# Optimization experiments

Measured on AMD Instinct MI355X. Metric: run time of the kernel, lower is better.

The kernel has to match this reference:

```python
import jax, jax.numpy as jnp
import numpy as np

N_NODES = 50000
IN_CH = 128
OUT_CH = 64
HID = 2 * OUT_CH  # 128
N_EDGES = 800000


def _glorot(key, shape):
    fan_in, fan_out = shape[0], shape[-1]
    lim = jnp.sqrt(6.0 / (fan_in + fan_out))
    return jax.random.uniform(key, shape, jnp.float32, -lim, lim)


def setup_inputs() -> dict:
    key = jax.random.key(0)
    ks = jax.random.split(key, 10)
    x = jax.random.normal(ks[0], (N_NODES, IN_CH), jnp.float32)
    edge_index = jax.random.randint(ks[1], (2, N_EDGES), 0, N_NODES, jnp.int32)
    return {
        "x": x,
        "edge_index": edge_index,
        "W1": _glorot(ks[2], (IN_CH, HID)),
        "a_src1": _glorot(ks[3], (HID,)),
        "a_dst1": _glorot(ks[4], (HID,)),
        "b1": jnp.zeros((HID,), jnp.float32),
        "W2": _glorot(ks[5], (HID, OUT_CH)),
        "a_src2": _glorot(ks[6], (OUT_CH,)),
        "a_dst2": _glorot(ks[7], (OUT_CH,)),
        "b2": jnp.zeros((OUT_CH,), jnp.float32),
    }


def _gat_conv(x, src, dst, W, a_src, a_dst, b, n_nodes):
    # Linear transform: [N, F_out]
    h = x @ W
    # Per-node attention halves (heads=1): alpha_i = <h_i, a>
    al_s = h @ a_src  # [N]
    al_d = h @ a_dst  # [N]
    # Edge scores with LeakyReLU(0.2), PyG default negative slope
    e = jax.nn.leaky_relu(al_s[src] + al_d[dst], negative_slope=0.2)
    # Segment softmax over incoming edges of each dst node
    m = jax.ops.segment_max(e, dst, num_segments=n_nodes)
    m = jnp.where(jnp.isfinite(m), m, 0.0)
    ex = jnp.exp(e - m[dst])
    denom = jax.ops.segment_sum(ex, dst, num_segments=n_nodes)
    alpha = ex / (denom[dst] + 1e-16)  # [E]
    # Weighted scatter-add aggregation
    out = jax.ops.segment_sum(h[src] * alpha[:, None], dst, num_segments=n_nodes)
    return out + b


def reference(x, edge_index, W1, a_src1, a_dst1, b1, W2, a_src2, a_dst2, b2):
    n = x.shape[0]
    # add_self_loops=True (PyG GATConv default)
    loops = jnp.arange(n, dtype=edge_index.dtype)
    src = jnp.concatenate([edge_index[0], loops])
    dst = jnp.concatenate([edge_index[1], loops])
    h = _gat_conv(x.astype(jnp.float32), src, dst, W1, a_src1, a_dst1, b1, n)
    h = jax.nn.relu(h)
    return _gat_conv(h, src, dst, W2, a_src2, a_dst2, b2, n)
```

## Files before the change

kernel.cpp:

```cpp
#include <hip/hip_runtime.h>
#include <hip/hip_bf16.h>

#define N_NODES 50000
#define IN_CH 128
#define HID 128
#define OUT_CH 64
#define N_EDGES 800000
#define N_TOT_EDGES (N_EDGES + N_NODES)
#define ET_PAD (N_TOT_EDGES + 3 * N_NODES)
#define MPAD 50048
#define NBN ((N_NODES + 255) / 256)
#define NB_E ((N_EDGES + 255) / 256)
#define NB_ET ((N_TOT_EDGES + 255) / 256)
#define NB_GEMM (MPAD / 64)
#define NB8 ((8 * N_NODES + 255) / 256)

typedef float float4v __attribute__((ext_vector_type(4)));
typedef unsigned uint4v __attribute__((ext_vector_type(4)));
typedef __attribute__((ext_vector_type(8))) short bf16x8;
typedef __attribute__((ext_vector_type(4))) float f32x4;

__device__ __forceinline__ unsigned bf16_rne(float f) {
    unsigned u = __float_as_uint(f);
    return (u + 0x7fffu + ((u >> 16) & 1u)) >> 16;
}
__device__ __forceinline__ unsigned pack2(float a, float b) {
    return bf16_rne(a) | (bf16_rne(b) << 16);
}

__global__ __launch_bounds__(256) void k_pre(
        int* __restrict__ cnt8,
        const float* __restrict__ W1, unsigned short* __restrict__ Wl1,
        const float* __restrict__ W2, unsigned short* __restrict__ Wl2) {
    const int b = blockIdx.x, t = threadIdx.x;
    if (b < NB8) {
        int i = b * 256 + t;
        if (i < 8 * N_NODES) cnt8[i] = 0;
        return;
    }
    const float* W; unsigned short* Wl; int N, bb;
    if (b < NB8 + 8) { W = W1; Wl = Wl1; N = 128; bb = b - NB8; }
    else             { W = W2; Wl = Wl2; N = 64;  bb = b - NB8 - 8; }
    const int tg = bb * 256 + t;
    if (tg >= 16 * N) return;
    const int kg = tg / N, col = tg & (N - 1);
    float v[8];
    #pragma unroll
    for (int j = 0; j < 8; ++j) v[j] = W[(size_t)(kg * 8 + j) * N + col];
    uint4 p;
    p.x = pack2(v[0], v[1]); p.y = pack2(v[2], v[3]);
    p.z = pack2(v[4], v[5]); p.w = pack2(v[6], v[7]);
    *(uint4*)&Wl[(size_t)tg * 8] = p;
}


__device__ __forceinline__ void count_body(int b, int t,
        const int* __restrict__ dst_row, int* __restrict__ cnt8,
        unsigned short* __restrict__ rank, int e) {
    int i = b * 256 + t;
    if (i < e) {
        int d = __builtin_nontemporal_load(&dst_row[i]);
        int c = b & 7;
        rank[i] = (unsigned short)atomicAdd(&cnt8[c * N_NODES + d], 1);
    }
}

template<int N, bool AF32, bool USELDS>
__device__ __forceinline__ void gemm_body(int gb, int t,
        const float* __restrict__ Xf, const unsigned short* __restrict__ Xb,
        const unsigned short* __restrict__ Wlg,
        const float* __restrict__ asrc, const float* __restrict__ adst,
        unsigned short* __restrict__ Hb, float* __restrict__ als,
        float* __restrict__ ald, int M, unsigned short* Wl) {
    constexpr int NF = N / 16;
    const unsigned short* Wsrc;
    if constexpr (USELDS) {
        for (int i = t; i < N * 16; i += 256)
            ((uint4*)Wl)[i] = ((const uint4*)Wlg)[i];
        __syncthreads();
        Wsrc = Wl;
    } else {
        Wsrc = Wlg;
    }

    const int lane = t & 63, w = t >> 6;
    const int rb = gb * 64 + w * 16;
    const int cl = lane & 15, g = lane >> 4;

    f32x4 acc[NF];
    #pragma unroll
    for (int n = 0; n < NF; ++n) acc[n] = (f32x4){0.f, 0.f, 0.f, 0.f};

    const float* Xrow = nullptr;
    const unsigned short* Abase = nullptr;
    if constexpr (AF32) {
        const int arow = (rb + cl < M) ? (rb + cl) : (M - 1);
        Xrow = Xf + (size_t)arow * 128;
    } else {
        Abase = Xb + (size_t)(rb >> 4) * 2048 + cl * 8;
    }

    #pragma unroll
    for (int s = 0; s < 4; ++s) {
        bf16x8 af;
        if constexpr (AF32) {
            const int k0 = (s * 4 + g) * 8;
            float4 a = *(const float4*)&Xrow[k0];
            float4 c = *(const float4*)&Xrow[k0 + 4];
            uint4v uu;
            uu[0] = pack2(a.x, a.y); uu[1] = pack2(a.z, a.w);
            uu[2] = pack2(c.x, c.y); uu[3] = pack2(c.z, c.w);
            af = __builtin_bit_cast(bf16x8, uu);
        } else {
            af = *(const bf16x8*)(Abase + (s * 4 + g) * 128);
        }
        #pragma unroll
        for (int n = 0; n < NF; ++n) {
            bf16x8 bf = *(const bf16x8*)(Wsrc + ((s * 4 + g) * N + n * 16 + cl) * 8);
            acc[n] = __builtin_amdgcn_mfma_f32_16x16x32_bf16(af, bf, acc[n], 0, 0, 0);
        }
    }

    float asv[NF], adv[NF];
    #pragma unroll
    for (int n = 0; n < NF; ++n) {
        asv[n] = asrc[n * 16 + cl];
        adv[n] = adst[n * 16 + cl];
    }

    #pragma unroll
    for (int r = 0; r < 4; ++r) {
        float ps = 0.f, pd = 0.f;
        #pragma unroll
        for (int n = 0; n < NF; ++n) {
            ps += acc[n][r] * asv[n];
            pd += acc[n][r] * adv[n];
        }
        #pragma unroll
        for (int mask = 1; mask < 16; mask <<= 1) {
            ps += __shfl_xor(ps, mask);
            pd += __shfl_xor(pd, mask);
        }
        const int row = rb + g * 4 + r;
        if (cl == 0 && row < M) { als[row] = ps; ald[row] = pd; }
    }

    #pragma unroll
    for (int r = 0; r < 4; ++r) {
        const int row = rb + g * 4 + r;
        if (row >= M) continue;
        #pragma unroll
        for (int n = 0; n < NF; ++n)
            Hb[(size_t)(n >> 1) * (size_t)M * 32 + (size_t)row * 32
               + (n & 1) * 16 + cl] = (unsigned short)bf16_rne(acc[n][r]);
    }
}

__global__ __launch_bounds__(256) void k_par1(
        const int* __restrict__ ei, int* __restrict__ cnt8,
        unsigned short* __restrict__ rank,
        const float* __restrict__ X, const unsigned short* __restrict__ Wl1,
        const float* __restrict__ asrc, const float* __restrict__ adst,
        unsigned short* __restrict__ Hb, float* __restrict__ als,
        float* __restrict__ ald, int M) {
    const int b = blockIdx.x, t = threadIdx.x;
    if (b < NB_E) { count_body(b, t, ei + N_EDGES, cnt8, rank, N_EDGES); return; }
    gemm_body<HID, true, false>(b - NB_E, t, X, nullptr, Wl1,
                                asrc, adst, Hb, als, ald, M, nullptr);
}

__global__ void k_scan1(const int* __restrict__ cnt8, int* __restrict__ cntT,
                        unsigned short* __restrict__ pcoff,
                        int* __restrict__ off, int* __restrict__ bsum, int n) {
    __shared__ int s[256];
    int t = threadIdx.x;
    int i = blockIdx.x * 256 + t;
    int padded = 0;
    if (i < n) {
        int pc = 1;
        unsigned short po[8];
        #pragma unroll
        for (int c = 0; c < 8; ++c) {
            po[c] = (unsigned short)pc;
            pc += cnt8[c * n + i];
        }
        cntT[i] = pc;
        uint4 p;
        p.x = (unsigned)po[0] | ((unsigned)po[1] << 16);
        p.y = (unsigned)po[2] | ((unsigned)po[3] << 16);
        p.z = (unsigned)po[4] | ((unsigned)po[5] << 16);
        p.w = (unsigned)po[6] | ((unsigned)po[7] << 16);
        *(uint4*)&pcoff[(size_t)i * 8] = p;
        padded = (pc + 3) & ~3;
    }
    s[t] = padded;
    __syncthreads();
    for (int d = 1; d < 256; d <<= 1) {
        int x = (t >= d) ? s[t - d] : 0;
        __syncthreads();
        s[t] += x;
        __syncthreads();
    }
    if (i < n) off[i + 1] = s[t];
    if (t == 255) bsum[blockIdx.x] = s[255];
}

__global__ void k_scan3(int* __restrict__ off, const int* __restrict__ bsum, int n) {
    __shared__ int s[256];
    int t = threadIdx.x;
    s[t] = (t < NBN) ? bsum[t] : 0;
    __syncthreads();
    for (int d = 1; d < 256; d <<= 1) {
        int x = (t >= d) ? s[t - d] : 0;
        __syncthreads();
        s[t] += x;
        __syncthreads();
    }
    int base = (blockIdx.x > 0) ? s[blockIdx.x - 1] : 0;
    int i = blockIdx.x * 256 + t;
    if (i < n) off[i + 1] += base;
    if (i == 0) off[0] = 0;
}

__global__ void k_fill2(const int* __restrict__ ei, const int* __restrict__ off,
                        const unsigned short* __restrict__ rank,
                        const unsigned short* __restrict__ pcoff,
                        int* __restrict__ csr, int e, int n) {
    int i = blockIdx.x * 256 + threadIdx.x;
    if (i < e) {
        int src = __builtin_nontemporal_load(&ei[i]);
        int dst = __builtin_nontemporal_load(&ei[e + i]);
        int c = (i >> 8) & 7;
        int pos = off[dst] + (int)pcoff[(size_t)dst * 8 + c] + (int)rank[i];
        csr[pos] = src;
    } else if (i < e + n) {
        int v = i - e;
        csr[off[v]] = v;
    }
}

__global__ __launch_bounds__(256) void gemm_mfma64(
        const unsigned short* __restrict__ Xb, const unsigned short* __restrict__ Wlg,
        const float* __restrict__ asrc, const float* __restrict__ adst,
        unsigned short* __restrict__ Hb, float* __restrict__ als,
        float* __restrict__ ald, int M) {
    __shared__ unsigned short Wl[16 * 64 * 8];
    gemm_body<OUT_CH, false, true>(blockIdx.x, threadIdx.x, nullptr, Xb, Wlg,
                                   asrc, adst, Hb, als, ald, M, Wl);
}

template<bool PADZ>
__global__ __launch_bounds__(256) void k_edgew(
        const float* __restrict__ als, const float* __restrict__ ald,
        const int* __restrict__ off, const int* __restrict__ cntT,
        const int* __restrict__ csr,
        unsigned* __restrict__ ew, float* __restrict__ invden, int n) {
    const int fl = threadIdx.x & 15;
    const int v = blockIdx.x * 16 + (threadIdx.x >> 4);
    if (v >= n) return;
    const int start = off[v], end = start + cntT[v];
    const float aldv = ald[v];
    float s = 0.f;
    for (int j = start + fl; j < end; j += 16) {
        int src = __builtin_nontemporal_load(&csr[j]);
        float e = als[src] + aldv;
        e = e > 0.f ? e : 0.2f * e;
        unsigned r = bf16_rne(__expf(e));
        ew[j] = ((unsigned)src << 16) | r;
        s += __uint_as_float(r << 16);
    }
    if (PADZ) {
        const int pend = off[v + 1];
        for (int j = end + fl; j < pend; j += 16) ew[j] = 0;
    }
    #pragma unroll
    for (int d = 1; d < 16; d <<= 1) s += __shfl_xor(s, d);
    if (fl == 0) invden[v] = 1.f / (s + 1e-16f);
}

template<int F, bool RELU, bool PACKOUT>
__global__ __launch_bounds__(256) void k_spmm_b(
        const unsigned short* __restrict__ Hb, const unsigned* __restrict__ ew,
        const float* __restrict__ invden, const float* __restrict__ bias,
        const int* __restrict__ off, void* __restrict__ outv, int n) {
    constexpr int NCH = F / 32;
    const int chunk = blockIdx.x % NCH;
    const int v = (blockIdx.x / NCH) * 64 + (threadIdx.x >> 2);
    if (v >= n) return;
    const int q = threadIdx.x & 3;
    const int start = off[v], end = off[v + 1];
    const unsigned short* __restrict__ Hch = Hb + (size_t)chunk * (size_t)n * 32 + q * 8;

    float a0[8] = {}, a1[8] = {}, a2[8] = {}, a3[8] = {};

    #define GATB(E, A)                                                   \
        {                                                                \
            float w_ = __uint_as_float((E) << 16);                       \
            uint4 h_ = *(const uint4*)&Hch[(size_t)((E) >> 16) * 32];    \
            A[0] += w_ * __uint_as_float(h_.x << 16);                    \
            A[1] += w_ * __uint_as_float(h_.x & 0xffff0000u);            \
            A[2] += w_ * __uint_as_float(h_.y << 16);                    \
            A[3] += w_ * __uint_as_float(h_.y & 0xffff0000u);            \
            A[4] += w_ * __uint_as_float(h_.z << 16);                    \
            A[5] += w_ * __uint_as_float(h_.z & 0xffff0000u);            \
            A[6] += w_ * __uint_as_float(h_.w << 16);                    \
            A[7] += w_ * __uint_as_float(h_.w & 0xffff0000u);            \
        }
    #define GATB4(Q) GATB((Q).x, a0) GATB((Q).y, a1) GATB((Q).z, a2) GATB((Q).w, a3)

    int j = start;
    for (; j + 4 < end; j += 8) {
        uint4 eA = *(const uint4*)&ew[j];
        uint4 eB = *(const uint4*)&ew[j + 4];
        GATB4(eA)
        GATB4(eB)
    }
    if (j < end) {
        uint4 eA = *(const uint4*)&ew[j];
        GATB4(eA)
    }
    #undef GATB4
    #undef GATB

    const float inv = invden[v];
    const float* __restrict__ bp = bias + chunk * 32 + q * 8;
    float s[8];
    #pragma unroll
    for (int i = 0; i < 8; ++i) {
        s[i] = (a0[i] + a1[i] + a2[i] + a3[i]) * inv + bp[i];
        if (RELU) s[i] = fmaxf(s[i], 0.f);
    }

    if (PACKOUT) {
        unsigned short* Xb2 = (unsigned short*)outv;
        const int kg = chunk * 4 + q;
        uint4v p;
        p[0] = pack2(s[0], s[1]); p[1] = pack2(s[2], s[3]);
        p[2] = pack2(s[4], s[5]); p[3] = pack2(s[6], s[7]);
        __builtin_nontemporal_store(p,
            (uint4v*)&Xb2[(size_t)(v >> 4) * 2048 + kg * 128 + (v & 15) * 8]);
    } else {
        float* out = (float*)outv;
        float4v o0, o1;
        o0[0] = s[0]; o0[1] = s[1]; o0[2] = s[2]; o0[3] = s[3];
        o1[0] = s[4]; o1[1] = s[5]; o1[2] = s[6]; o1[3] = s[7];
        float* op = out + (size_t)v * F + chunk * 32 + q * 8;
        __builtin_nontemporal_store(o0, (float4v*)op);
        __builtin_nontemporal_store(o1, (float4v*)(op + 4));
    }
}


extern "C" void kernel_launch(void* const* d_in, const int* in_sizes, int n_in,
                              void* d_out, int out_size, void* d_ws, size_t ws_size,
                              hipStream_t stream) {
    const float* x     = (const float*)d_in[0];
    const int*   ei    = (const int*)d_in[1];
    const float* W1    = (const float*)d_in[2];
    const float* as1   = (const float*)d_in[3];
    const float* ad1   = (const float*)d_in[4];
    const float* b1    = (const float*)d_in[5];
    const float* W2    = (const float*)d_in[6];
    const float* as2   = (const float*)d_in[7];
    const float* ad2   = (const float*)d_in[8];
    const float* b2    = (const float*)d_in[9];
    float* out = (float*)d_out;

    const int Nn = N_NODES;

    char* ws = (char*)d_ws;
    size_t o = 0;
    auto carve = [&](size_t bytes) { char* p = ws + o; o = (o + bytes + 255) & ~(size_t)255; return p; };
    int*            off  = (int*)carve((Nn + 1) * sizeof(int));
    int*            cnt8 = (int*)carve((size_t)8 * Nn * sizeof(int));
    int*            cntT = (int*)carve(Nn * sizeof(int));
    int*            bsum = (int*)carve(256 * sizeof(int));
    unsigned short* rank = (unsigned short*)carve((size_t)N_EDGES * sizeof(unsigned short));
    unsigned short* pcoff= (unsigned short*)carve((size_t)Nn * 8 * sizeof(unsigned short));
    int*            csr  = (int*)carve((size_t)ET_PAD * sizeof(int));
    unsigned*       ew   = (unsigned*)carve((size_t)ET_PAD * sizeof(unsigned));
    unsigned short* h1b  = (unsigned short*)carve((size_t)Nn * HID * sizeof(unsigned short));
    unsigned short* h2b  = (unsigned short*)carve((size_t)Nn * OUT_CH * sizeof(unsigned short));
    unsigned short* Xb2  = (unsigned short*)carve((size_t)MPAD * 128 * sizeof(unsigned short));
    unsigned short* Wl1  = (unsigned short*)carve(16 * 128 * 8 * sizeof(unsigned short));
    unsigned short* Wl2  = (unsigned short*)carve(16 * 64 * 8 * sizeof(unsigned short));
    float*          als  = (float*)carve(Nn * sizeof(float));
    float*          ald  = (float*)carve(Nn * sizeof(float));
    float*          invd = (float*)carve(Nn * sizeof(float));

    k_pre<<<NB8 + 12, 256, 0, stream>>>(cnt8, W1, Wl1, W2, Wl2);

    k_par1<<<NB_E + NB_GEMM, 256, 0, stream>>>(
        ei, cnt8, rank, x, Wl1, as1, ad1, h1b, als, ald, Nn);

    k_scan1<<<NBN, 256, 0, stream>>>(cnt8, cntT, pcoff, off, bsum, Nn);
    k_scan3<<<NBN, 256, 0, stream>>>(off, bsum, Nn);

    k_fill2<<<NB_ET, 256, 0, stream>>>(ei, off, rank, pcoff, csr, N_EDGES, Nn);

    const int nbEW  = (Nn + 15) / 16;
    const int nbN64 = (Nn + 63) / 64;

    k_edgew<true><<<nbEW, 256, 0, stream>>>(als, ald, off, cntT, csr, ew, invd, Nn);
    k_spmm_b<HID, true, true><<<nbN64 * (HID / 32), 256, 0, stream>>>(
        h1b, ew, invd, b1, off, Xb2, Nn);

    gemm_mfma64<<<NB_GEMM, 256, 0, stream>>>(
        Xb2, Wl2, as2, ad2, h2b, als, ald, Nn);
    k_edgew<false><<<nbEW, 256, 0, stream>>>(als, ald, off, cntT, csr, ew, invd, Nn);
    k_spmm_b<OUT_CH, false, false><<<nbN64 * (OUT_CH / 32), 256, 0, stream>>>(
        h2b, ew, invd, b2, off, out, Nn);
}
```

Baseline: 164.4 us.

## Replace global atomic degree counting with per-shard LDS byte-packed histograms

Edge in-degree counting now runs in 128 shards. Each shard builds a histogram in shared memory, packing four 8-bit counters per dword, and writes it to a per-shard count array. This removes the global atomics on cnt8 and the zero-init pass, and shrinks the rank and prefix-offset arrays to bytes. In exchange the scan kernel loops serially over 128 shards per node, and the 8-bit counters assume no node gets more than 255 edges within one shard.

```diff
diff --git a/kernel.cpp b/kernel.cpp
--- a/kernel.cpp
+++ b/kernel.cpp
@@ -10,10 +10,11 @@
 #define ET_PAD (N_TOT_EDGES + 3 * N_NODES)
 #define MPAD 50048
 #define NBN ((N_NODES + 255) / 256)
-#define NB_E ((N_EDGES + 255) / 256)
 #define NB_ET ((N_TOT_EDGES + 255) / 256)
 #define NB_GEMM (MPAD / 64)
-#define NB8 ((8 * N_NODES + 255) / 256)
+#define NSH 128
+#define EPS (N_EDGES / NSH)
+#define NDW (N_NODES / 4)
 
 typedef float float4v __attribute__((ext_vector_type(4)));
 typedef unsigned uint4v __attribute__((ext_vector_type(4)));
@@ -29,18 +30,12 @@
 }
 
 __global__ __launch_bounds__(256) void k_pre(
-        int* __restrict__ cnt8,
         const float* __restrict__ W1, unsigned short* __restrict__ Wl1,
         const float* __restrict__ W2, unsigned short* __restrict__ Wl2) {
     const int b = blockIdx.x, t = threadIdx.x;
-    if (b < NB8) {
-        int i = b * 256 + t;
-        if (i < 8 * N_NODES) cnt8[i] = 0;
-        return;
-    }
     const float* W; unsigned short* Wl; int N, bb;
-    if (b < NB8 + 8) { W = W1; Wl = Wl1; N = 128; bb = b - NB8; }
-    else             { W = W2; Wl = Wl2; N = 64;  bb = b - NB8 - 8; }
+    if (b < 8) { W = W1; Wl = Wl1; N = 128; bb = b; }
+    else       { W = W2; Wl = Wl2; N = 64;  bb = b - 8; }
     const int tg = bb * 256 + t;
     if (tg >= 16 * N) return;
     const int kg = tg / N, col = tg & (N - 1);
@@ -51,18 +46,6 @@
     p.x = pack2(v[0], v[1]); p.y = pack2(v[2], v[3]);
     p.z = pack2(v[4], v[5]); p.w = pack2(v[6], v[7]);
     *(uint4*)&Wl[(size_t)tg * 8] = p;
-}
-
-
-__device__ __forceinline__ void count_body(int b, int t,
-        const int* __restrict__ dst_row, int* __restrict__ cnt8,
-        unsigned short* __restrict__ rank, int e) {
-    int i = b * 256 + t;
-    if (i < e) {
-        int d = __builtin_nontemporal_load(&dst_row[i]);
-        int c = b & 7;
-        rank[i] = (unsigned short)atomicAdd(&cnt8[c * N_NODES + d], 1);
-    }
 }
 
 template<int N, bool AF32, bool USELDS>
@@ -157,40 +140,51 @@
 }
 
 __global__ __launch_bounds__(256) void k_par1(
-        const int* __restrict__ ei, int* __restrict__ cnt8,
-        unsigned short* __restrict__ rank,
+        const int* __restrict__ ei, unsigned* __restrict__ cnt_s,
+        unsigned char* __restrict__ rank8,
         const float* __restrict__ X, const unsigned short* __restrict__ Wl1,
         const float* __restrict__ asrc, const float* __restrict__ adst,
         unsigned short* __restrict__ Hb, float* __restrict__ als,
         float* __restrict__ ald, int M) {
+    __shared__ unsigned lcnt[NDW];
     const int b = blockIdx.x, t = threadIdx.x;
-    if (b < NB_E) { count_body(b, t, ei + N_EDGES, cnt8, rank, N_EDGES); return; }
-    gemm_body<HID, true, false>(b - NB_E, t, X, nullptr, Wl1,
+    if (b < NSH) {
+        const int s = b;
+        for (int i = t; i < NDW; i += 256) lcnt[i] = 0;
+        __syncthreads();
+        const int base = s * EPS;
+        const int* __restrict__ dst = ei + N_EDGES;
+        for (int j = base + t; j < base + EPS; j += 256) {
+            int d = __builtin_nontemporal_load(&dst[j]);
+            unsigned sh = 8u * (d & 3);
+            unsigned old = atomicAdd(&lcnt[d >> 2], 1u << sh);
+            rank8[j] = (unsigned char)((old >> sh) & 0xFFu);
+        }
+        __syncthreads();
+        unsigned* __restrict__ outp = cnt_s + (size_t)s * NDW;
+        for (int i = t; i < NDW; i += 256) outp[i] = lcnt[i];
+        return;
+    }
+    gemm_body<HID, true, false>(b - NSH, t, X, nullptr, Wl1,
                                 asrc, adst, Hb, als, ald, M, nullptr);
 }
 
-__global__ void k_scan1(const int* __restrict__ cnt8, int* __restrict__ cntT,
-                        unsigned short* __restrict__ pcoff,
+__global__ void k_scan1(const unsigned* __restrict__ cnt_s, int* __restrict__ cntT,
+                        unsigned char* __restrict__ pcoff8,
                         int* __restrict__ off, int* __restrict__ bsum, int n) {
     __shared__ int s[256];
     int t = threadIdx.x;
     int i = blockIdx.x * 256 + t;
     int padded = 0;
     if (i < n) {
+        const int dw = i >> 2;
+        const unsigned sh = 8u * (i & 3);
         int pc = 1;
-        unsigned short po[8];
-        #pragma unroll
-        for (int c = 0; c < 8; ++c) {
-            po[c] = (unsigned short)pc;
-            pc += cnt8[c * n + i];
+        for (int c = 0; c < NSH; ++c) {
+            pcoff8[(size_t)c * n + i] = (unsigned char)pc;
+            pc += (int)((cnt_s[(size_t)c * NDW + dw] >> sh) & 0xFFu);
         }
         cntT[i] = pc;
-        uint4 p;
-        p.x = (unsigned)po[0] | ((unsigned)po[1] << 16);
-        p.y = (unsigned)po[2] | ((unsigned)po[3] << 16);
-        p.z = (unsigned)po[4] | ((unsigned)po[5] << 16);
-        p.w = (unsigned)po[6] | ((unsigned)po[7] << 16);
-        *(uint4*)&pcoff[(size_t)i * 8] = p;
         padded = (pc + 3) & ~3;
     }
     s[t] = padded;
@@ -223,15 +217,15 @@
 }
 
 __global__ void k_fill2(const int* __restrict__ ei, const int* __restrict__ off,
-                        const unsigned short* __restrict__ rank,
-                        const unsigned short* __restrict__ pcoff,
+                        const unsigned char* __restrict__ rank8,
+                        const unsigned char* __restrict__ pcoff8,
                         int* __restrict__ csr, int e, int n) {
     int i = blockIdx.x * 256 + threadIdx.x;
     if (i < e) {
         int src = __builtin_nontemporal_load(&ei[i]);
         int dst = __builtin_nontemporal_load(&ei[e + i]);
-        int c = (i >> 8) & 7;
-        int pos = off[dst] + (int)pcoff[(size_t)dst * 8 + c] + (int)rank[i];
+        int c = i / EPS;
+        int pos = off[dst] + (int)pcoff8[(size_t)c * n + dst] + (int)rank8[i];
         csr[pos] = src;
     } else if (i < e + n) {
         int v = i - e;
@@ -371,32 +365,32 @@
     char* ws = (char*)d_ws;
     size_t o = 0;
     auto carve = [&](size_t bytes) { char* p = ws + o; o = (o + bytes + 255) & ~(size_t)255; return p; };
-    int*            off  = (int*)carve((Nn + 1) * sizeof(int));
-    int*            cnt8 = (int*)carve((size_t)8 * Nn * sizeof(int));
-    int*            cntT = (int*)carve(Nn * sizeof(int));
-    int*            bsum = (int*)carve(256 * sizeof(int));
-    unsigned short* rank = (unsigned short*)carve((size_t)N_EDGES * sizeof(unsigned short));
-    unsigned short* pcoff= (unsigned short*)carve((size_t)Nn * 8 * sizeof(unsigned short));
-    int*            csr  = (int*)carve((size_t)ET_PAD * sizeof(int));
-    unsigned*       ew   = (unsigned*)carve((size_t)ET_PAD * sizeof(unsigned));
-    unsigned short* h1b  = (unsigned short*)carve((size_t)Nn * HID * sizeof(unsigned short));
-    unsigned short* h2b  = (unsigned short*)carve((size_t)Nn * OUT_CH * sizeof(unsigned short));
-    unsigned short* Xb2  = (unsigned short*)carve((size_t)MPAD * 128 * sizeof(unsigned short));
-    unsigned short* Wl1  = (unsigned short*)carve(16 * 128 * 8 * sizeof(unsigned short));
-    unsigned short* Wl2  = (unsigned short*)carve(16 * 64 * 8 * sizeof(unsigned short));
-    float*          als  = (float*)carve(Nn * sizeof(float));
-    float*          ald  = (float*)carve(Nn * sizeof(float));
-    float*          invd = (float*)carve(Nn * sizeof(float));
-
-    k_pre<<<NB8 + 12, 256, 0, stream>>>(cnt8, W1, Wl1, W2, Wl2);
-
-    k_par1<<<NB_E + NB_GEMM, 256, 0, stream>>>(
-        ei, cnt8, rank, x, Wl1, as1, ad1, h1b, als, ald, Nn);
-
-    k_scan1<<<NBN, 256, 0, stream>>>(cnt8, cntT, pcoff, off, bsum, Nn);
+    int*            off   = (int*)carve((Nn + 1) * sizeof(int));
+    int*            cntT  = (int*)carve(Nn * sizeof(int));
+    int*            bsum  = (int*)carve(256 * sizeof(int));
+    unsigned char*  rank8 = (unsigned char*)carve((size_t)N_EDGES);
+    unsigned*       cnt_s = (unsigned*)carve((size_t)NSH * NDW * sizeof(unsigned));
+    unsigned char*  pcoff8= (unsigned char*)carve((size_t)NSH * Nn);
+    int*            csr   = (int*)carve((size_t)ET_PAD * sizeof(int));
+    unsigned*       ew    = (unsigned*)carve((size_t)ET_PAD * sizeof(unsigned));
+    unsigned short* h1b   = (unsigned short*)carve((size_t)Nn * HID * sizeof(unsigned short));
+    unsigned short* h2b   = (unsigned short*)carve((size_t)Nn * OUT_CH * sizeof(unsigned short));
+    unsigned short* Xb2   = (unsigned short*)carve((size_t)MPAD * 128 * sizeof(unsigned short));
+    unsigned short* Wl1   = (unsigned short*)carve(16 * 128 * 8 * sizeof(unsigned short));
+    unsigned short* Wl2   = (unsigned short*)carve(16 * 64 * 8 * sizeof(unsigned short));
+    float*          als   = (float*)carve(Nn * sizeof(float));
+    float*          ald   = (float*)carve(Nn * sizeof(float));
+    float*          invd  = (float*)carve(Nn * sizeof(float));
+
+    k_pre<<<12, 256, 0, stream>>>(W1, Wl1, W2, Wl2);
+
+    k_par1<<<NSH + NB_GEMM, 256, 0, stream>>>(
+        ei, cnt_s, rank8, x, Wl1, as1, ad1, h1b, als, ald, Nn);
+
+    k_scan1<<<NBN, 256, 0, stream>>>(cnt_s, cntT, pcoff8, off, bsum, Nn);
     k_scan3<<<NBN, 256, 0, stream>>>(off, bsum, Nn);
 
-    k_fill2<<<NB_ET, 256, 0, stream>>>(ei, off, rank, pcoff, csr, N_EDGES, Nn);
+    k_fill2<<<NB_ET, 256, 0, stream>>>(ei, off, rank8, pcoff8, csr, N_EDGES, Nn);
 
     const int nbEW  = (Nn + 15) / 16;
     const int nbN64 = (Nn + 63) / 64;
```

Result: faster. 152.3 us (-7.3%).
